# Kernel tuning notes

Hardware: AMD Instinct MI355X
Metric: run time of the kernel (lower is better)

## Reference

```python
import jax, jax.numpy as jnp
import numpy as np

EMB = 1024
HEADS = 16
HEAD_SIZE = EMB // HEADS


def setup_inputs() -> dict:
    key = jax.random.key(0)
    ks = jax.random.split(key, 10)
    s = 1.0 / np.sqrt(EMB)
    return {
        "x": jax.random.normal(ks[0], (2, 2048, EMB), dtype=jnp.float32),
        "ln_gamma": jnp.ones((EMB,), jnp.float32),
        "ln_beta": jnp.zeros((EMB,), jnp.float32),
        "Wq": jax.random.normal(ks[1], (EMB, EMB), jnp.float32) * s,
        "bq": jnp.zeros((EMB,), jnp.float32),
        "Wk": jax.random.normal(ks[2], (EMB, EMB), jnp.float32) * s,
        "bk": jnp.zeros((EMB,), jnp.float32),
        "Wv": jax.random.normal(ks[3], (EMB, EMB), jnp.float32) * s,
        "bv": jnp.zeros((EMB,), jnp.float32),
        "Wo": jax.random.normal(ks[4], (EMB, EMB), jnp.float32) * s,
        "bo": jnpps if False else jnp.zeros((EMB,), jnp.float32),
    }


def _layernorm(x, gamma, beta, eps=1e-5):
    mu = jnp.mean(x, axis=-1, keepdims=True)
    var = jnp.mean(jnp.square(x - mu), axis=-1, keepdims=True)
    return (x - mu) * jax.lax.rsqrt(var + eps) * gamma + beta


def reference(x, ln_gamma, ln_beta, Wq, bq, Wk, bk, Wv, bv, Wo, bo):
    B, L, D = x.shape
    h = _layernorm(x, ln_gamma, ln_beta)
    # projections -> [B, H, L, hd]
    def split_heads(t):
        return t.reshape(B, L, HEADS, HEAD_SIZE).transpose(0, 2, 1, 3)
    q = split_heads(h @ Wq.T + bq)
    k = split_heads(h @ Wk.T + bk)
    v = split_heads(h @ Wv.T + bv)
    scale = HEAD_SIZE ** (-0.5)
    w = jnp.einsum("bhqd,bhkd->bhqk", q, k) * scale  # [B,H,L,L]
    w = jax.nn.softmax(w, axis=-1)
    o = jnp.einsum("bhqk,bhkd->bhqd", w, v)
    o = o.transpose(0, 2, 1, 3).reshape(B, L, D)
    o = o @ Wo.T + bo
    return x + o
```

## Files before the change

### kernel.cpp

```cpp
#include <hip/hip_runtime.h>
#include <math.h>

#define B_   2
#define L_   2048
#define EMB_ 1024
#define H_   16
#define HD_  64
#define M_   (B_ * L_)
#define KSPLIT 2
#define LOG2E 1.44269504088896f

typedef __bf16 bf16x8 __attribute__((ext_vector_type(8)));
typedef __bf16 bf16x4 __attribute__((ext_vector_type(4)));
typedef __bf16 bf16x2 __attribute__((ext_vector_type(2)));
typedef float floatx16 __attribute__((ext_vector_type(16)));
typedef unsigned int uintx2 __attribute__((ext_vector_type(2)));

typedef __attribute__((address_space(1))) const void GV;
typedef __attribute__((address_space(3))) void LV;

#define MFMA32(a, b, c) __builtin_amdgcn_mfma_f32_32x32x16_bf16((a), (b), (c), 0, 0, 0)

#if __has_builtin(__builtin_amdgcn_exp2f)
#define EXP2(x) __builtin_amdgcn_exp2f(x)
#else
#define EXP2(x) exp2f(x)
#endif

#define SWZ(row) ((((row) & 7) ^ (((row) >> 3) & 3)))

__device__ __forceinline__ int pkbf(float a, float b) {
#if __has_builtin(__builtin_amdgcn_cvt_pk_bf16_f32)
    union { bf16x2 v; int i; } u;
    u.v = __builtin_amdgcn_cvt_pk_bf16_f32(a, b);
    return u.i;
#else
    union { __bf16 h[2]; int i; } u;
    u.h[0] = (__bf16)a; u.h[1] = (__bf16)b;
    return u.i;
#endif
}

__global__ __launch_bounds__(256) void prep_kernel(
        const float* __restrict__ x, const float* __restrict__ gamma,
        const float* __restrict__ beta, __bf16* __restrict__ h,
        const float* __restrict__ s0, const float* __restrict__ s1,
        const float* __restrict__ s2, const float* __restrict__ s3,
        __bf16* __restrict__ d0, __bf16* __restrict__ d1,
        __bf16* __restrict__ d2, __bf16* __restrict__ d3) {
    int bid = blockIdx.x;
    int tid = threadIdx.x;
    if (bid >= M_) {
        int wb = bid - M_;
        int z = wb >> 8;
        const float* s = (z == 0) ? s0 : (z == 1) ? s1 : (z == 2) ? s2 : s3;
        __bf16* d = (z == 0) ? d0 : (z == 1) ? d1 : (z == 2) ? d2 : d3;
        size_t base = (size_t)((wb & 255) * 256 + tid) * 16;
#pragma unroll
        for (int j = 0; j < 4; ++j) {
            float4 f = *(const float4*)(s + base + j * 4);
            bf16x4 t;
            t[0] = (__bf16)f.x; t[1] = (__bf16)f.y; t[2] = (__bf16)f.z; t[3] = (__bf16)f.w;
            *(bf16x4*)(d + base + j * 4) = t;
        }
        return;
    }
    int row = bid;
    const float* xr = x + (size_t)row * EMB_;
    float4 v = *(const float4*)(xr + tid * 4);
    float s  = v.x + v.y + v.z + v.w;
    float ss = v.x * v.x + v.y * v.y + v.z * v.z + v.w * v.w;
    for (int off = 32; off; off >>= 1) {
        s  += __shfl_down(s, off, 64);
        ss += __shfl_down(ss, off, 64);
    }
    __shared__ float s1_[4], s2_[4];
    int wid = tid >> 6;
    if ((tid & 63) == 0) { s1_[wid] = s; s2_[wid] = ss; }
    __syncthreads();
    if (tid == 0) {
        float a = s1_[0] + s1_[1] + s1_[2] + s1_[3];
        float b = s2_[0] + s2_[1] + s2_[2] + s2_[3];
        float mu = a / EMB_;
        float var = b / EMB_ - mu * mu;
        s1_[0] = mu;
        s2_[0] = rsqrtf(var + 1e-5f);
    }
    __syncthreads();
    float mu = s1_[0], rstd = s2_[0];
    float4 g4 = *(const float4*)(gamma + tid * 4);
    float4 b4 = *(const float4*)(beta + tid * 4);
    bf16x4 o;
    o[0] = (__bf16)((v.x - mu) * rstd * g4.x + b4.x);
    o[1] = (__bf16)((v.y - mu) * rstd * g4.y + b4.y);
    o[2] = (__bf16)((v.z - mu) * rstd * g4.z + b4.z);
    o[3] = (__bf16)((v.w - mu) * rstd * g4.w + b4.w);
    *(bf16x4*)(h + (size_t)row * EMB_ + tid * 4) = o;
}

__device__ __forceinline__ void stage_tile128(const __bf16* gbase, __bf16* lds,
                                              int wave, int lane) {
    int srow = lane >> 3;
    int gch0 = lane & 7;
#pragma unroll
    for (int s = 0; s < 4; ++s) {
        int seg = wave * 4 + s;
        int row = seg * 8 + srow;
        int g = gch0 ^ SWZ(row);
        __builtin_amdgcn_global_load_lds(
            (GV*)(gbase + (size_t)row * EMB_ + g * 8),
            (LV*)(lds + seg * 512 + lane * 8), 16, 0, 0);
    }
}

__global__ __launch_bounds__(256) void gemm_qkv_mfma(
        const __bf16* __restrict__ A, const __bf16* __restrict__ W,
        const float* __restrict__ bq, const float* __restrict__ bk,
        const float* __restrict__ bv,
        __bf16* __restrict__ Qo, __bf16* __restrict__ Ko,
        __bf16* __restrict__ Vto) {
    __shared__ __bf16 As[128 * 64];
    __shared__ __bf16 Bs[128 * 64];
    int tid = threadIdx.x, wave = tid >> 6, lane = tid & 63;
    int wm = wave >> 1, wn = wave & 1;
    int quad = lane >> 5, lq = lane & 31;
    int flat = blockIdx.y * gridDim.x + blockIdx.x;
    int nf = (flat & 7) * 96 + (flat >> 3);
    int bm = (nf / 24) * 128, bn = (nf % 24) * 128;

    floatx16 acc[2][2];
#pragma unroll
    for (int i = 0; i < 2; ++i)
#pragma unroll
        for (int j = 0; j < 2; ++j)
#pragma unroll
            for (int r = 0; r < 16; ++r) acc[i][j][r] = 0.f;

    for (int k0 = 0; k0 < EMB_; k0 += 64) {
        __syncthreads();
        stage_tile128(A + (size_t)bm * EMB_ + k0, As, wave, lane);
        stage_tile128(W + (size_t)bn * EMB_ + k0, Bs, wave, lane);
        __syncthreads();
#pragma unroll
        for (int s = 0; s < 4; ++s) {
            int g = 2 * s + quad;
            int r0 = wm * 64 + lq, r1 = r0 + 32;
            int c0 = wn * 64 + lq, c1 = c0 + 32;
            bf16x8 a0 = *(const bf16x8*)&As[r0 * 64 + ((g ^ SWZ(r0)) * 8)];
            bf16x8 a1 = *(const bf16x8*)&As[r1 * 64 + ((g ^ SWZ(r1)) * 8)];
            bf16x8 b0 = *(const bf16x8*)&Bs[c0 * 64 + ((g ^ SWZ(c0)) * 8)];
            bf16x8 b1 = *(const bf16x8*)&Bs[c1 * 64 + ((g ^ SWZ(c1)) * 8)];
            acc[0][0] = MFMA32(a0, b0, acc[0][0]);
            acc[0][1] = MFMA32(a0, b1, acc[0][1]);
            acc[1][0] = MFMA32(a1, b0, acc[1][0]);
            acc[1][1] = MFMA32(a1, b1, acc[1][1]);
        }
    }

#pragma unroll
    for (int mb = 0; mb < 2; ++mb) {
#pragma unroll
        for (int nb = 0; nb < 2; ++nb) {
            int col = bn + wn * 64 + nb * 32 + lq;
            int z = col >> 10;
            int cc = col & 1023;
            float bv_ = (z == 0) ? bq[cc] : (z == 1) ? bk[cc] : bv[cc];
            if (z < 2) {
                __bf16* dst = (z == 0) ? Qo : Ko;
                float qs = (z == 0) ? 0.125f * LOG2E : 1.0f;
#pragma unroll
                for (int r = 0; r < 16; ++r) {
                    int row = bm + wm * 64 + mb * 32 + (r & 3) + 8 * (r >> 2) + 4 * quad;
                    dst[(size_t)row * EMB_ + cc] = (__bf16)((acc[mb][nb][r] + bv_) * qs);
                }
            } else {
                int hh = cc >> 6, d = cc & 63;
#pragma unroll
                for (int rb = 0; rb < 4; ++rb) {
                    int row = bm + wm * 64 + mb * 32 + 8 * rb + 4 * quad;
                    int b = row >> 11, l = row & (L_ - 1);
                    bf16x4 t;
#pragma unroll
                    for (int a = 0; a < 4; ++a) t[a] = (__bf16)(acc[mb][nb][4 * rb + a] + bv_);
                    *(bf16x4*)(Vto + ((size_t)(b * H_ + hh) * HD_ + d) * L_ + l) = t;
                }
            }
        }
    }
}

__global__ __launch_bounds__(256) void gemm_out_mfma(
        const __bf16* __restrict__ A, const __bf16* __restrict__ W,
        const float* __restrict__ bias, const float* __restrict__ x,
        float* __restrict__ out) {
    __shared__ __bf16 As[128 * 64];
    __shared__ __bf16 Bs[128 * 64];
    int tid = threadIdx.x, wave = tid >> 6, lane = tid & 63;
    int wm = wave >> 1, wn = wave & 1;
    int quad = lane >> 5, lq = lane & 31;
    int flat = blockIdx.y * gridDim.x + blockIdx.x;
    int nf = (flat & 7) * 32 + (flat >> 3);
    int bm = (nf / 8) * 128, bn = (nf % 8) * 128;

    floatx16 acc[2][2];
#pragma unroll
    for (int i = 0; i < 2; ++i)
#pragma unroll
        for (int j = 0; j < 2; ++j)
#pragma unroll
            for (int r = 0; r < 16; ++r) acc[i][j][r] = 0.f;

    for (int k0 = 0; k0 < EMB_; k0 += 64) {
        __syncthreads();
        stage_tile128(A + (size_t)bm * EMB_ + k0, As, wave, lane);
        stage_tile128(W + (size_t)bn * EMB_ + k0, Bs, wave, lane);
        __syncthreads();
#pragma unroll
        for (int s = 0; s < 4; ++s) {
            int g = 2 * s + quad;
            int r0 = wm * 64 + lq, r1 = r0 + 32;
            int c0 = wn * 64 + lq, c1 = c0 + 32;
            bf16x8 a0 = *(const bf16x8*)&As[r0 * 64 + ((g ^ SWZ(r0)) * 8)];
            bf16x8 a1 = *(const bf16x8*)&As[r1 * 64 + ((g ^ SWZ(r1)) * 8)];
            bf16x8 b0 = *(const bf16x8*)&Bs[c0 * 64 + ((g ^ SWZ(c0)) * 8)];
            bf16x8 b1 = *(const bf16x8*)&Bs[c1 * 64 + ((g ^ SWZ(c1)) * 8)];
            acc[0][0] = MFMA32(a0, b0, acc[0][0]);
            acc[0][1] = MFMA32(a0, b1, acc[0][1]);
            acc[1][0] = MFMA32(a1, b0, acc[1][0]);
            acc[1][1] = MFMA32(a1, b1, acc[1][1]);
        }
    }

#pragma unroll
    for (int mb = 0; mb < 2; ++mb) {
#pragma unroll
        for (int nb = 0; nb < 2; ++nb) {
            int col = bn + wn * 64 + nb * 32 + lq;
            float bv_ = bias[col];
#pragma unroll
            for (int r = 0; r < 16; ++r) {
                size_t row = bm + wm * 64 + mb * 32 + (r & 3) + 8 * (r >> 2) + 4 * quad;
                out[row * EMB_ + col] = acc[mb][nb][r] + bv_ + x[row * EMB_ + col];
            }
        }
    }
}

__global__ __launch_bounds__(512, 2) void attn_mfma(
        const __bf16* __restrict__ Q,
        const __bf16* __restrict__ K,
        const __bf16* __restrict__ Vt,
        __bf16* __restrict__ Op,
        float* __restrict__ Lp) {
    __shared__ __bf16 Ks[2][64 * 64];
    __shared__ __bf16 Vs[2][64 * 64];

    int tid = threadIdx.x, wave = tid >> 6, lane = tid & 63;
    int quad = lane >> 5, lq = lane & 31;
    int bh = blockIdx.x;
    int ks = blockIdx.z;
    int b = bh >> 4, h = bh & 15;
    int q0 = blockIdx.y * 256 + wave * 32;
    const size_t tok0 = (size_t)b * L_;

    const __bf16* Kb = K + tok0 * EMB_ + h * HD_;
    const __bf16* Vb = Vt + (size_t)bh * HD_ * L_;

    bf16x8 qf[4];
    {
        const __bf16* qp = Q + (tok0 + q0 + lq) * EMB_ + h * HD_ + quad * 8;
#pragma unroll
        for (int s = 0; s < 4; ++s) qf[s] = *(const bf16x8*)(qp + s * 16);
    }

    floatx16 oacc[2];
#pragma unroll
    for (int j = 0; j < 2; ++j)
#pragma unroll
        for (int r = 0; r < 16; ++r) oacc[j][r] = 0.f;
    float lacc = 0.f;

    int srow = lane >> 3, gch0 = lane & 7;

    auto stage = [&](int buf, int kt) {
        int row = wave * 8 + srow;
        int g = gch0 ^ SWZ(row);
        __builtin_amdgcn_global_load_lds(
            (GV*)(Kb + (size_t)(kt + row) * EMB_ + g * 8),
            (LV*)(&Ks[buf][wave * 512 + lane * 8]), 16, 0, 0);
        __builtin_amdgcn_global_load_lds(
            (GV*)(Vb + (size_t)row * L_ + kt + g * 8),
            (LV*)(&Vs[buf][wave * 512 + lane * 8]), 16, 0, 0);
    };

    auto compute = [&](int buf) {
#pragma unroll
        for (int nb = 0; nb < 2; ++nb) {
            int krow = nb * 32 + lq;
            bf16x8 kf[4];
#pragma unroll
            for (int s = 0; s < 4; ++s)
                kf[s] = *(const bf16x8*)&Ks[buf][krow * 64 + (((2 * s + quad) ^ SWZ(krow)) * 8)];

            floatx16 sacc;
#pragma unroll
            for (int r = 0; r < 16; ++r) sacc[r] = 0.f;
            __builtin_amdgcn_s_setprio(1);
#pragma unroll
            for (int s = 0; s < 4; ++s) sacc = MFMA32(kf[s], qf[s], sacc);
            __builtin_amdgcn_s_setprio(0);

            int P[8];
            float lsum = 0.f;
#pragma unroll
            for (int t = 0; t < 8; ++t) {
                float pa = EXP2(sacc[2 * t]);
                float pb = EXP2(sacc[2 * t + 1]);
                lsum += pa + pb;
                P[t] = pkbf(pa, pb);
            }
            lacc += lsum;
            union { int i[4]; bf16x8 v; } bf0, bf1;
#if __has_builtin(__builtin_amdgcn_permlane32_swap)
            {
                uintx2 r;
                r = __builtin_amdgcn_permlane32_swap((unsigned)P[0], (unsigned)P[2], false, false);
                bf0.i[0] = (int)r[0]; bf0.i[2] = (int)r[1];
                r = __builtin_amdgcn_permlane32_swap((unsigned)P[1], (unsigned)P[3], false, false);
                bf0.i[1] = (int)r[0]; bf0.i[3] = (int)r[1];
                r = __builtin_amdgcn_permlane32_swap((unsigned)P[4], (unsigned)P[6], false, false);
                bf1.i[0] = (int)r[0]; bf1.i[2] = (int)r[1];
                r = __builtin_amdgcn_permlane32_swap((unsigned)P[5], (unsigned)P[7], false, false);
                bf1.i[1] = (int)r[0]; bf1.i[3] = (int)r[1];
            }
#else
            int X[8];
#pragma unroll
            for (int t = 0; t < 8; ++t) X[t] = __shfl_xor(P[t], 32, 64);
            bf0.i[0] = quad ? X[2] : P[0];
            bf0.i[1] = quad ? X[3] : P[1];
            bf0.i[2] = quad ? P[2] : X[0];
            bf0.i[3] = quad ? P[3] : X[1];
            bf1.i[0] = quad ? X[6] : P[4];
            bf1.i[1] = quad ? X[7] : P[5];
            bf1.i[2] = quad ? P[6] : X[4];
            bf1.i[3] = quad ? P[7] : X[5];
#endif

            __builtin_amdgcn_s_setprio(1);
#pragma unroll
            for (int half = 0; half < 2; ++half) {
                int t = 2 * nb + half;
#pragma unroll
                for (int db = 0; db < 2; ++db) {
                    int drow = db * 32 + lq;
                    bf16x8 vf = *(const bf16x8*)&Vs[buf][drow * 64 + (((2 * t + quad) ^ SWZ(drow)) * 8)];
                    oacc[db] = MFMA32(vf, half ? bf1.v : bf0.v, oacc[db]);
                }
            }
            __builtin_amdgcn_s_setprio(0);
        }
    };

    const int kt0 = ks * (L_ / KSPLIT);
    const int NT = (L_ / KSPLIT) / 64;

    stage(0, kt0);
    for (int t = 0; t < NT; ++t) {
        __syncthreads();
        if (t + 1 < NT) stage((t + 1) & 1, kt0 + (t + 1) * 64);
        compute(t & 1);
    }

    {
        float l = lacc + __shfl_xor(lacc, 32, 64);
        if (lane < 32)
            Lp[((size_t)ks * 32 + bh) * L_ + q0 + lane] = l;
    }
#pragma unroll
    for (int db = 0; db < 2; ++db)
#pragma unroll
        for (int r = 0; r < 16; ++r) {
            int dp = db * 32 + (r & 3) + 8 * (r >> 2) + 4 * quad;
            Op[((size_t)(ks * 32 + bh) * HD_ + dp) * L_ + q0 + lq] =
                (__bf16)oacc[db][r];
        }
}

__global__ __launch_bounds__(256) void combine_kernel(
        const __bf16* __restrict__ Op, const float* __restrict__ Lp,
        __bf16* __restrict__ Ob) {
    __shared__ float lrl[64];
    __shared__ __bf16 T[64][72];
    int t = threadIdx.x;
    int qt = blockIdx.x * 64;
    int bh = blockIdx.y;
    int b = bh >> 4, h = bh & 15;

    if (t < 64) {
        float l = 0.f;
#pragma unroll
        for (int ks = 0; ks < KSPLIT; ++ks)
            l += Lp[((size_t)ks * 32 + bh) * L_ + qt + t];
        lrl[t] = 1.0f / l;
    }
    __syncthreads();

#pragma unroll
    for (int cc = 0; cc < 2; ++cc) {
        int id = t + cc * 256;
        int d = id >> 3, q8 = (id & 7) * 8;
        float acc[8];
#pragma unroll
        for (int j = 0; j < 8; ++j) acc[j] = 0.f;
#pragma unroll
        for (int ks = 0; ks < KSPLIT; ++ks) {
            bf16x8 v = *(const bf16x8*)(Op + ((size_t)(ks * 32 + bh) * HD_ + d) * L_ + qt + q8);
#pragma unroll
            for (int j = 0; j < 8; ++j) acc[j] += (float)v[j];
        }
#pragma unroll
        for (int j = 0; j < 8; ++j)
            T[q8 + j][d] = (__bf16)(acc[j] * lrl[q8 + j]);
    }
    __syncthreads();

#pragma unroll
    for (int cc = 0; cc < 2; ++cc) {
        int id = t + cc * 256;
        int tl = id >> 3, dc = (id & 7) * 8;
        bf16x8 v = *(const bf16x8*)&T[tl][dc];
        *(bf16x8*)(Ob + ((size_t)b * L_ + qt + tl) * EMB_ + h * HD_ + dc) = v;
    }
}

extern "C" void kernel_launch(void* const* d_in, const int* in_sizes, int n_in,
                              void* d_out, int out_size, void* d_ws, size_t ws_size,
                              hipStream_t stream) {
    const float* x     = (const float*)d_in[0];
    const float* gamma = (const float*)d_in[1];
    const float* beta  = (const float*)d_in[2];
    const float* Wq    = (const float*)d_in[3];
    const float* bq    = (const float*)d_in[4];
    const float* Wk    = (const float*)d_in[5];
    const float* bk    = (const float*)d_in[6];
    const float* Wv    = (const float*)d_in[7];
    const float* bv    = (const float*)d_in[8];
    const float* Wo    = (const float*)d_in[9];
    const float* bo    = (const float*)d_in[10];
    float* out = (float*)d_out;

    const size_t SLAB = (size_t)M_ * EMB_;
    const size_t WSLAB = (size_t)EMB_ * EMB_;
    char* ws = (char*)d_ws;
    __bf16* hb    = (__bf16*)ws;                      ws += SLAB * 2;
    __bf16* Qb    = (__bf16*)ws;                      ws += SLAB * 2;
    __bf16* Kb    = (__bf16*)ws;                      ws += SLAB * 2;
    __bf16* Vtb   = (__bf16*)ws;                      ws += SLAB * 2;
    __bf16* Wqkvb = (__bf16*)ws;                      ws += 3 * WSLAB * 2;
    __bf16* Wob   = (__bf16*)ws;                      ws += WSLAB * 2;
    __bf16* Op    = (__bf16*)ws;                      ws += (size_t)KSPLIT * SLAB * 2;
    float*  Lp    = (float*)ws;                       ws += (size_t)KSPLIT * 32 * L_ * 4;
    __bf16* Ob    = hb;

    prep_kernel<<<M_ + 1024, 256, 0, stream>>>(
        x, gamma, beta, hb,
        Wq, Wk, Wv, Wo, Wqkvb, Wqkvb + WSLAB, Wqkvb + 2 * WSLAB, Wob);
    gemm_qkv_mfma<<<dim3(3 * EMB_ / 128, M_ / 128), 256, 0, stream>>>(
        hb, Wqkvb, bq, bk, bv, Qb, Kb, Vtb);
    attn_mfma<<<dim3(B_ * H_, L_ / 256, KSPLIT), 512, 0, stream>>>(Qb, Kb, Vtb, Op, Lp);
    combine_kernel<<<dim3(L_ / 64, B_ * H_), 256, 0, stream>>>(Op, Lp, Ob);
    gemm_out_mfma<<<dim3(EMB_ / 128, M_ / 128), 256, 0, stream>>>(Ob, Wob, bo, x, out);
}
```

Baseline: 199.1 us.

## Fuse split-K combine into a second sequential attention launch

Replaces the grid-level key split plus separate combine kernel with two launches of the attention kernel, each covering half the keys. The second launch adds the first half's partial output and row sum, normalizes, transposes through shared memory and writes the token-major output directly. This removes the combine kernel and its extra global traffic. In exchange, each launch has half the blocks, which lowers parallelism, and the two key halves now run serially.

```diff
diff --git a/kernel.cpp b/kernel.cpp
--- a/kernel.cpp
+++ b/kernel.cpp
@@ -251,14 +251,17 @@
         const __bf16* __restrict__ K,
         const __bf16* __restrict__ Vt,
         __bf16* __restrict__ Op,
-        float* __restrict__ Lp) {
-    __shared__ __bf16 Ks[2][64 * 64];
-    __shared__ __bf16 Vs[2][64 * 64];
+        float* __restrict__ Lp,
+        __bf16* __restrict__ Ob,
+        int ks, int fin) {
+    __shared__ __bf16 smem[18432];
+    __bf16* KsB = smem;
+    __bf16* VsB = smem + 8192;
+    __bf16* Tsm = smem;
 
     int tid = threadIdx.x, wave = tid >> 6, lane = tid & 63;
     int quad = lane >> 5, lq = lane & 31;
     int bh = blockIdx.x;
-    int ks = blockIdx.z;
     int b = bh >> 4, h = bh & 15;
     int q0 = blockIdx.y * 256 + wave * 32;
     const size_t tok0 = (size_t)b * L_;
@@ -287,10 +290,10 @@
         int g = gch0 ^ SWZ(row);
         __builtin_amdgcn_global_load_lds(
             (GV*)(Kb + (size_t)(kt + row) * EMB_ + g * 8),
-            (LV*)(&Ks[buf][wave * 512 + lane * 8]), 16, 0, 0);
+            (LV*)(KsB + buf * 4096 + wave * 512 + lane * 8), 16, 0, 0);
         __builtin_amdgcn_global_load_lds(
             (GV*)(Vb + (size_t)row * L_ + kt + g * 8),
-            (LV*)(&Vs[buf][wave * 512 + lane * 8]), 16, 0, 0);
+            (LV*)(VsB + buf * 4096 + wave * 512 + lane * 8), 16, 0, 0);
     };
 
     auto compute = [&](int buf) {
@@ -300,7 +303,7 @@
             bf16x8 kf[4];
 #pragma unroll
             for (int s = 0; s < 4; ++s)
-                kf[s] = *(const bf16x8*)&Ks[buf][krow * 64 + (((2 * s + quad) ^ SWZ(krow)) * 8)];
+                kf[s] = *(const bf16x8*)(KsB + buf * 4096 + krow * 64 + (((2 * s + quad) ^ SWZ(krow)) * 8));
 
             floatx16 sacc;
 #pragma unroll
@@ -354,7 +357,7 @@
 #pragma unroll
                 for (int db = 0; db < 2; ++db) {
                     int drow = db * 32 + lq;
-                    bf16x8 vf = *(const bf16x8*)&Vs[buf][drow * 64 + (((2 * t + quad) ^ SWZ(drow)) * 8)];
+                    bf16x8 vf = *(const bf16x8*)(VsB + buf * 4096 + drow * 64 + (((2 * t + quad) ^ SWZ(drow)) * 8));
                     oacc[db] = MFMA32(vf, half ? bf1.v : bf0.v, oacc[db]);
                 }
             }
@@ -372,65 +375,38 @@
         compute(t & 1);
     }
 
-    {
-        float l = lacc + __shfl_xor(lacc, 32, 64);
+    float l = lacc + __shfl_xor(lacc, 32, 64);
+    if (!fin) {
         if (lane < 32)
-            Lp[((size_t)ks * 32 + bh) * L_ + q0 + lane] = l;
-    }
-#pragma unroll
-    for (int db = 0; db < 2; ++db)
-#pragma unroll
-        for (int r = 0; r < 16; ++r) {
-            int dp = db * 32 + (r & 3) + 8 * (r >> 2) + 4 * quad;
-            Op[((size_t)(ks * 32 + bh) * HD_ + dp) * L_ + q0 + lq] =
-                (__bf16)oacc[db][r];
-        }
-}
-
-__global__ __launch_bounds__(256) void combine_kernel(
-        const __bf16* __restrict__ Op, const float* __restrict__ Lp,
-        __bf16* __restrict__ Ob) {
-    __shared__ float lrl[64];
-    __shared__ __bf16 T[64][72];
-    int t = threadIdx.x;
-    int qt = blockIdx.x * 64;
-    int bh = blockIdx.y;
-    int b = bh >> 4, h = bh & 15;
-
-    if (t < 64) {
-        float l = 0.f;
-#pragma unroll
-        for (int ks = 0; ks < KSPLIT; ++ks)
-            l += Lp[((size_t)ks * 32 + bh) * L_ + qt + t];
-        lrl[t] = 1.0f / l;
-    }
-    __syncthreads();
-
-#pragma unroll
-    for (int cc = 0; cc < 2; ++cc) {
-        int id = t + cc * 256;
-        int d = id >> 3, q8 = (id & 7) * 8;
-        float acc[8];
-#pragma unroll
-        for (int j = 0; j < 8; ++j) acc[j] = 0.f;
-#pragma unroll
-        for (int ks = 0; ks < KSPLIT; ++ks) {
-            bf16x8 v = *(const bf16x8*)(Op + ((size_t)(ks * 32 + bh) * HD_ + d) * L_ + qt + q8);
-#pragma unroll
-            for (int j = 0; j < 8; ++j) acc[j] += (float)v[j];
-        }
-#pragma unroll
-        for (int j = 0; j < 8; ++j)
-            T[q8 + j][d] = (__bf16)(acc[j] * lrl[q8 + j]);
-    }
-    __syncthreads();
-
-#pragma unroll
-    for (int cc = 0; cc < 2; ++cc) {
-        int id = t + cc * 256;
-        int tl = id >> 3, dc = (id & 7) * 8;
-        bf16x8 v = *(const bf16x8*)&T[tl][dc];
-        *(bf16x8*)(Ob + ((size_t)b * L_ + qt + tl) * EMB_ + h * HD_ + dc) = v;
+            Lp[(size_t)bh * L_ + q0 + lane] = l;
+#pragma unroll
+        for (int db = 0; db < 2; ++db)
+#pragma unroll
+            for (int r = 0; r < 16; ++r) {
+                int dp = db * 32 + (r & 3) + 8 * (r >> 2) + 4 * quad;
+                Op[((size_t)bh * HD_ + dp) * L_ + q0 + lq] = (__bf16)oacc[db][r];
+            }
+    } else {
+        l += Lp[(size_t)bh * L_ + q0 + lq];
+        float rl = 1.0f / l;
+        __syncthreads();
+        int qloc = wave * 32 + lq;
+#pragma unroll
+        for (int db = 0; db < 2; ++db)
+#pragma unroll
+            for (int r = 0; r < 16; ++r) {
+                int dp = db * 32 + (r & 3) + 8 * (r >> 2) + 4 * quad;
+                float p0 = (float)Op[((size_t)bh * HD_ + dp) * L_ + q0 + lq];
+                Tsm[qloc * 72 + dp] = (__bf16)((oacc[db][r] + p0) * rl);
+            }
+        __syncthreads();
+        int qblk = blockIdx.y * 256;
+#pragma unroll
+        for (int cc = 0; cc < 4; ++cc) {
+            int tl = cc * 64 + (tid >> 3), dc = (tid & 7) * 8;
+            bf16x8 v = *(const bf16x8*)&Tsm[tl * 72 + dc];
+            *(bf16x8*)(Ob + ((size_t)b * L_ + qblk + tl) * EMB_ + h * HD_ + dc) = v;
+        }
     }
 }
 
@@ -468,7 +444,10 @@
         Wq, Wk, Wv, Wo, Wqkvb, Wqkvb + WSLAB, Wqkvb + 2 * WSLAB, Wob);
     gemm_qkv_mfma<<<dim3(3 * EMB_ / 128, M_ / 128), 256, 0, stream>>>(
         hb, Wqkvb, bq, bk, bv, Qb, Kb, Vtb);
-    attn_mfma<<<dim3(B_ * H_, L_ / 256, KSPLIT), 512, 0, stream>>>(Qb, Kb, Vtb, Op, Lp);
-    combine_kernel<<<dim3(L_ / 64, B_ * H_), 256, 0, stream>>>(Op, Lp, Ob);
-    gemm_out_mfma<<<dim3(EMB_ / 128, M_ / 128), 256, 0, stream>>>(Ob, Wob, bo, x, out);
-}
+    attn_mfma<<<dim3(B_ * H_, L_ / 256), 512, 0, stream>>>(
+        Qb, Kb, Vtb, Op, Lp, Ob, 0, 0);
+    attn_mfma<<<dim3(B_ * H_, L_ / 256), 512, 0, stream>>>(
+        Qb, Kb, Vtb, Op, Lp, Ob, 1, 1);
+    gemm_out_mfma<<<dim3(EMB_ / 128, M_ / 128), 256, 0, stream>>>(
+        Ob, Wob, bo, x, out);
+}
```

Measured after the change: 193.1 us. 1.03x faster.
